# Kernel tuning notes

Measured on AMD Instinct MI355X. Metric: run time of the kernel, lower is better.

## Reference

```python
import jax, jax.numpy as jnp
import numpy as np

# NTU-25 joint groupings (0-indexed)
BODY_GROUP = [np.array([5,6,7,8,22,23])-1, np.array([9,10,11,12,24,25])-1,
              np.array([13,14,15,16])-1, np.array([17,18,19,20])-1,
              np.array([1,2,3,4,21])-1]
PART_GROUP = [np.array([1,2,21])-1, np.array([3,4])-1, np.array([5,6,7])-1,
              np.array([8,22,23])-1, np.array([9,10,11])-1, np.array([12,24,25])-1,
              np.array([13,14])-1, np.array([15,16])-1, np.array([17,18])-1,
              np.array([19,20])-1]

def _corr_joints(parts):
    num_joints = max(max(p) for p in parts) + 1
    res = []
    for i in range(num_joints):
        for j, p in enumerate(parts):
            if i in p:
                res.append(j)
                break
    return np.asarray(res, dtype=np.int32)

JOINTS_PART = _corr_joints(PART_GROUP)  # [25] -> part id in [0,10)
JOINTS_BODY = _corr_joints(BODY_GROUP)  # [25] -> body id in [0,5)

N, C, T, V, S = 64, 96, 128, 25, 3

def setup_inputs() -> dict:
    key = jax.random.key(0)
    ks = jax.random.split(key, 10)
    x = jax.random.normal(ks[0], (N, C, T, V), jnp.float32)
    p_att = jax.random.normal(ks[1], (N, S, 10, 10), jnp.float32)
    b_att = jax.random.normal(ks[2], (N, S, 5, 5), jnp.float32)
    w_in = jax.random.normal(ks[3], (3 * C, C), jnp.float32) * (1.0 / np.sqrt(C))
    b_in = jax.random.normal(ks[4], (3 * C,), jnp.float32) * 0.01
    w_ff = jax.random.normal(ks[5], (C, C), jnp.float32) * (1.0 / np.sqrt(C))
    b_ff = jax.random.normal(ks[6], (C,), jnp.float32) * 0.01
    bn_gamma = jnp.ones((C,), jnp.float32)
    bn_beta = jnp.zeros((C,), jnp.float32)
    bn_mean = jnp.zeros((C,), jnp.float32)
    bn_var = jnp.ones((C,), jnp.float32)
    return {"x": x, "p_att": p_att, "b_att": b_att, "w_in": w_in, "b_in": b_in,
            "w_ff": w_ff, "b_ff": b_ff, "bn_gamma": bn_gamma, "bn_beta": bn_beta,
            "bn_mean": bn_mean, "bn_var": bn_var}

def reference(x, p_att, b_att, w_in, b_in, w_ff, b_ff, bn_gamma, bn_beta, bn_mean, bn_var):
    n, c, t, v = x.shape
    s = S
    mid = c // s
    jp = jnp.asarray(JOINTS_PART)
    jb = jnp.asarray(JOINTS_BODY)
    # 1x1 conv -> QKV: [N, 3C, T, V] viewed as [N, 3, S, mid, T, V]
    qkv = jnp.einsum('nctv,oc->notv', x, w_in) + b_in[None, :, None, None]
    qkv = qkv.reshape(n, 3, s, mid, t, v)
    q, k, val = qkv[:, 0], qkv[:, 1], qkv[:, 2]
    att = jnp.tanh(jnp.einsum('nsctu,nsctv->nsuv', q, k) / (mid * t))
    # structured gather of part/body biases to joint-level [N,S,V,V]
    pp = p_att[:, :, jp[:, None], jp[None, :]]
    bb = b_att[:, :, jb[:, None], jb[None, :]]
    att = att + pp + bb
    y = jnp.einsum('nsuv,nsctv->nsctu', att, val).reshape(n, c, t, v)
    # ff_nets: 1x1 conv + BatchNorm (eval mode, running stats)
    y = jnp.einsum('nctv,oc->notv', y, w_ff) + b_ff[None, :, None, None]
    inv = bn_gamma / jnp.sqrt(bn_var + 1e-5)
    y = (y - bn_mean[None, :, None, None]) * inv[None, :, None, None] + bn_beta[None, :, None, None]
    return jax.nn.leaky_relu(x + y, 0.1)
```

## Files before the change

kernel.cpp:

```cpp
#include <hip/hip_runtime.h>
#include <cmath>

#define NN 64
#define CC 96
#define TT 128
#define VV 25
#define SS 3
#define TB 4
#define NTB (TT/TB)
#define ROWS (TB*VV)
#define XTROWS 112

#define XTP 104
#define XFP 104
#define QKP 200
#define VALP 40
#define YLP 104

typedef __attribute__((ext_vector_type(8))) __bf16 bf16x8;
typedef __attribute__((ext_vector_type(4))) float f32x4;

#define MFMA16(a,b,c) __builtin_amdgcn_mfma_f32_16x16x32_bf16((a),(b),(c),0,0,0)

__constant__ int JP[25] = {0,0,1,1,2,2,2,3,4,4,4,5,6,6,7,7,8,8,9,9,0,3,3,5,5};
__constant__ int JB[25] = {4,4,4,4,0,0,0,0,1,1,1,1,2,2,2,2,3,3,3,3,4,0,0,1,1};

__device__ inline unsigned short f2b(float f) {
  unsigned int u = __float_as_uint(f);
  u += 0x7fffu + ((u >> 16) & 1u);
  return (unsigned short)(u >> 16);
}
__device__ inline float b2f(unsigned short h) {
  return __uint_as_float(((unsigned int)h) << 16);
}
__device__ inline bf16x8 ldbf8(const unsigned short* p) {
  union { uint4 u; bf16x8 b; } z;
  z.u = *(const uint4*)p;
  return z.b;
}
__device__ inline f32x4 fz() {
  f32x4 z; z[0] = 0.f; z[1] = 0.f; z[2] = 0.f; z[3] = 0.f; return z;
}

__global__ __launch_bounds__(256) void k0(
    const float* __restrict__ w_in, const float* __restrict__ w_ff,
    const float* __restrict__ b_ff, const float* __restrict__ gam,
    const float* __restrict__ bet, const float* __restrict__ mea,
    const float* __restrict__ var,
    unsigned short* __restrict__ wbin, unsigned short* __restrict__ wbff,
    float* __restrict__ scsh)
{
  int i = blockIdx.x * 256 + threadIdx.x;
  if (i < 288 * 96) wbin[i] = f2b(w_in[i]);
  if (i < 96 * 96)  wbff[i] = f2b(w_ff[i]);
  if (i < 96) {
    float sc = gam[i] * rsqrtf(var[i] + 1e-5f);
    scsh[i]      = sc;
    scsh[96 + i] = (b_ff[i] - mea[i]) * sc + bet[i];
  }
}

__device__ inline void stageA(const float* __restrict__ xb,
                              unsigned short* __restrict__ xf, int tid)
{
  for (int e = tid; e < CC * (ROWS / 4); e += 256) {
    int i4 = e % (ROWS / 4), c = e / (ROWS / 4);
    float4 v = *(const float4*)&xb[(size_t)c * (TT * VV) + i4 * 4];
    ushort4 h;
    h.x = f2b(v.x); h.y = f2b(v.y); h.z = f2b(v.z); h.w = f2b(v.w);
    *(ushort4*)&xf[c * XFP + i4 * 4] = h;
  }
}
__device__ inline void stageB(const unsigned short* __restrict__ xf,
                              unsigned short* __restrict__ xT, int tid)
{
  for (int e = tid; e < ROWS * (CC / 4); e += 256) {
    int i = e % ROWS, c4 = e / ROWS;
    ushort4 h;
    h.x = xf[(c4 * 4 + 0) * XFP + i];
    h.y = xf[(c4 * 4 + 1) * XFP + i];
    h.z = xf[(c4 * 4 + 2) * XFP + i];
    h.w = xf[(c4 * 4 + 3) * XFP + i];
    *(ushort4*)&xT[i * XTP + c4 * 4] = h;
  }
}

__global__ __launch_bounds__(256, 2) void k1(
    const float* __restrict__ x, const unsigned short* __restrict__ wbin,
    const float* __restrict__ b_in, float* __restrict__ partG)
{
  __shared__ __align__(16) unsigned short xT[XTROWS * XTP];
  __shared__ __align__(16) unsigned short qk[XTROWS * QKP];
  __shared__ float bL[192];
  unsigned short* xf = qk;

  const int tid  = threadIdx.x;
  const int wid  = tid >> 6, lane = tid & 63;
  const int lrow = lane & 15;
  const int lk8  = (lane >> 4) << 3;
  const int ldr4 = (lane >> 4) << 2;
  const int tb = blockIdx.x & (NTB - 1);
  const int n  = blockIdx.x >> 5;
  const int t0 = tb * TB;

  const float* xb = x + (size_t)n * CC * TT * VV + (size_t)t0 * VV;
  stageA(xb, xf, tid);
  if (tid < 192) bL[tid] = b_in[tid];
  __syncthreads();
  stageB(xf, xT, tid);
  __syncthreads();

  f32x4 acc[3][7];
  #pragma unroll
  for (int i = 0; i < 3; ++i)
    #pragma unroll
    for (int nf = 0; nf < 7; ++nf) acc[i][nf] = fz();

  #pragma unroll
  for (int ks = 0; ks < 3; ++ks) {
    bf16x8 a[3];
    #pragma unroll
    for (int i = 0; i < 3; ++i)
      a[i] = ldbf8(&wbin[((wid * 3 + i) * 16 + lrow) * 96 + ks * 32 + lk8]);
    #pragma unroll
    for (int nf = 0; nf < 7; ++nf) {
      bf16x8 b = ldbf8(&xT[(nf * 16 + lrow) * XTP + ks * 32 + lk8]);
      #pragma unroll
      for (int i = 0; i < 3; ++i)
        acc[i][nf] = MFMA16(a[i], b, acc[i][nf]);
    }
  }
  #pragma unroll
  for (int i = 0; i < 3; ++i) {
    int ob = (wid * 3 + i) * 16 + ldr4;
    float4 bb = *(const float4*)&bL[ob];
    #pragma unroll
    for (int nf = 0; nf < 7; ++nf) {
      int col = nf * 16 + lrow;
      ushort4 h;
      h.x = f2b(acc[i][nf][0] + bb.x);
      h.y = f2b(acc[i][nf][1] + bb.y);
      h.z = f2b(acc[i][nf][2] + bb.z);
      h.w = f2b(acc[i][nf][3] + bb.w);
      *(ushort4*)&qk[col * QKP + ob] = h;
    }
  }
  __syncthreads();

  if (wid < 3) {
    const int s = wid;
    f32x4 g[2][2];
    g[0][0] = fz(); g[0][1] = fz(); g[1][0] = fz(); g[1][1] = fz();
    #pragma unroll
    for (int dt = 0; dt < TB; ++dt) {
      int r0 = dt * VV;
      bf16x8 a0 = ldbf8(&qk[(r0 + lrow) * QKP + s * 32 + lk8]);
      bf16x8 a1 = ldbf8(&qk[(r0 + 16 + lrow) * QKP + s * 32 + lk8]);
      bf16x8 b0 = ldbf8(&qk[(r0 + lrow) * QKP + 96 + s * 32 + lk8]);
      bf16x8 b1 = ldbf8(&qk[(r0 + 16 + lrow) * QKP + 96 + s * 32 + lk8]);
      g[0][0] = MFMA16(a0, b0, g[0][0]);
      g[0][1] = MFMA16(a0, b1, g[0][1]);
      g[1][0] = MFMA16(a1, b0, g[1][0]);
      g[1][1] = MFMA16(a1, b1, g[1][1]);
    }
    float* pg = partG + ((size_t)tb * (NN * SS) + (n * SS + s)) * (VV * VV);
    #pragma unroll
    for (int mi = 0; mi < 2; ++mi)
      #pragma unroll
      for (int ni = 0; ni < 2; ++ni)
        #pragma unroll
        for (int r = 0; r < 4; ++r) {
          int u = mi * 16 + ldr4 + r, v = ni * 16 + lrow;
          if (u < VV && v < VV) pg[u * VV + v] = g[mi][ni][r];
        }
  }
}

__global__ __launch_bounds__(256) void k2(
    const float* __restrict__ partG, const float* __restrict__ p_att,
    const float* __restrict__ b_att, unsigned short* __restrict__ att)
{
  const int ns = blockIdx.x;
  for (int e = threadIdx.x; e < 1024; e += 256) {
    int u = e >> 5, v = e & 31;
    float a = 0.f;
    if (u < VV && v < VV) {
      float g = 0.f;
      #pragma unroll 4
      for (int tb = 0; tb < NTB; ++tb)
        g += partG[((size_t)tb * (NN * SS) + ns) * (VV * VV) + u * VV + v];
      a = tanhf(g * (1.0f / 4096.0f))
        + p_att[(size_t)ns * 100 + JP[u] * 10 + JP[v]]
        + b_att[(size_t)ns * 25  + JB[u] * 5  + JB[v]];
    }
    att[(size_t)ns * 1024 + e] = f2b(a);
  }
}

__global__ __launch_bounds__(256, 2) void k3(
    const float* __restrict__ x, const unsigned short* __restrict__ wbin,
    const unsigned short* __restrict__ wbff,
    const float* __restrict__ b_in, const float* __restrict__ scsh,
    const unsigned short* __restrict__ att, float* __restrict__ out)
{
  __shared__ __align__(16) unsigned short xT[XTROWS * XTP];
  __shared__ __align__(16) unsigned short val[384 * VALP];
  unsigned short* xf = val;

  const int tid  = threadIdx.x;
  const int wid  = tid >> 6, lane = tid & 63;
  const int lrow = lane & 15;
  const int lk8  = (lane >> 4) << 3;
  const int ldr4 = (lane >> 4) << 2;
  const int tb = blockIdx.x & (NTB - 1);
  const int n  = blockIdx.x >> 5;
  const int t0 = tb * TB;

  const float* xb = x + (size_t)n * CC * TT * VV + (size_t)t0 * VV;
  stageA(xb, xf, tid);
  __syncthreads();
  stageB(xf, xT, tid);
  __syncthreads();
  {
    uint4 z; z.x = 0u; z.y = 0u; z.z = 0u; z.w = 0u;
    for (int e = tid; e < 384; e += 256)
      *(uint4*)&val[e * VALP + 24] = z;
  }
  __syncthreads();

  for (int nf = wid * 2; nf < 7 && nf < wid * 2 + 2; ++nf) {
    f32x4 acc[6];
    #pragma unroll
    for (int mf = 0; mf < 6; ++mf) acc[mf] = fz();
    #pragma unroll
    for (int ks = 0; ks < 3; ++ks) {
      bf16x8 b = ldbf8(&xT[(nf * 16 + lrow) * XTP + ks * 32 + lk8]);
      #pragma unroll
      for (int mf = 0; mf < 6; ++mf) {
        bf16x8 a = ldbf8(&wbin[(192 + mf * 16 + lrow) * 96 + ks * 32 + lk8]);
        acc[mf] = MFMA16(a, b, acc[mf]);
      }
    }
    int col = nf * 16 + lrow;
    if (col < ROWS) {
      int dt = col / VV, v = col - dt * VV;
      #pragma unroll
      for (int mf = 0; mf < 6; ++mf) {
        float4 bb = *(const float4*)&b_in[192 + mf * 16 + ldr4];
        const float* bp = (const float*)&bb;
        #pragma unroll
        for (int r = 0; r < 4; ++r) {
          int c = mf * 16 + ldr4 + r;
          val[(dt * 96 + c) * VALP + v] = f2b(acc[mf][r] + bp[r]);
        }
      }
    }
  }
  __syncthreads();

  const unsigned short* attn = att + (size_t)(n * SS) * 1024;
  f32x4 y[3][2][2];
  #pragma unroll
  for (int s = 0; s < 3; ++s)
    #pragma unroll
    for (int mi = 0; mi < 2; ++mi)
      #pragma unroll
      for (int ci = 0; ci < 2; ++ci) y[s][mi][ci] = fz();

  #pragma unroll
  for (int s = 0; s < 3; ++s) {
    bf16x8 b[2];
    #pragma unroll
    for (int ci = 0; ci < 2; ++ci) {
      int col = (wid * 2 + ci) * 16 + lrow;
      int dt = col >> 5, cm = col & 31;
      b[ci] = ldbf8(&val[(dt * 96 + s * 32 + cm) * VALP + lk8]);
    }
    #pragma unroll
    for (int mi = 0; mi < 2; ++mi) {
      bf16x8 a = ldbf8(&attn[(size_t)s * 1024 + (mi * 16 + lrow) * 32 + lk8]);
      #pragma unroll
      for (int ci = 0; ci < 2; ++ci)
        y[s][mi][ci] = MFMA16(a, b[ci], y[s][mi][ci]);
    }
  }
  __syncthreads();

  unsigned short* yL = val;
  #pragma unroll
  for (int s = 0; s < 3; ++s)
    #pragma unroll
    for (int mi = 0; mi < 2; ++mi)
      #pragma unroll
      for (int ci = 0; ci < 2; ++ci) {
        int col = (wid * 2 + ci) * 16 + lrow;
        int dt = col >> 5, cm = col & 31;
        int c = s * 32 + cm;
        #pragma unroll
        for (int r = 0; r < 4; ++r) {
          int u = mi * 16 + ldr4 + r;
          if (u < VV) yL[(dt * VV + u) * YLP + c] = f2b(y[s][mi][ci][r]);
        }
      }
  __syncthreads();

  for (int nf = wid * 2; nf < 7 && nf < wid * 2 + 2; ++nf) {
    f32x4 acc[6];
    #pragma unroll
    for (int mf = 0; mf < 6; ++mf) acc[mf] = fz();
    #pragma unroll
    for (int ks = 0; ks < 3; ++ks) {
      bf16x8 b = ldbf8(&yL[(nf * 16 + lrow) * YLP + ks * 32 + lk8]);
      #pragma unroll
      for (int mf = 0; mf < 6; ++mf) {
        bf16x8 a = ldbf8(&wbff[(mf * 16 + lrow) * 96 + ks * 32 + lk8]);
        acc[mf] = MFMA16(a, b, acc[mf]);
      }
    }
    int i = nf * 16 + lrow;
    if (i < ROWS) {
      int dt = i / VV, u = i - dt * VV;
      int t = t0 + dt;
      #pragma unroll
      for (int mf = 0; mf < 6; ++mf) {
        int o0 = mf * 16 + ldr4;
        ushort4 xr = *(const ushort4*)&xT[i * XTP + o0];
        float4 sc = *(const float4*)&scsh[o0];
        float4 sh = *(const float4*)&scsh[96 + o0];
        float zr[4];
        zr[0] = acc[mf][0] * sc.x + sh.x + b2f(xr.x);
        zr[1] = acc[mf][1] * sc.y + sh.y + b2f(xr.y);
        zr[2] = acc[mf][2] * sc.z + sh.z + b2f(xr.z);
        zr[3] = acc[mf][3] * sc.w + sh.w + b2f(xr.w);
        #pragma unroll
        for (int r = 0; r < 4; ++r) {
          float z = zr[r];
          z = (z >= 0.f) ? z : 0.1f * z;
          out[((size_t)(n * CC + o0 + r) * TT + t) * VV + u] = z;
        }
      }
    }
  }
}

extern "C" void kernel_launch(void* const* d_in, const int* in_sizes, int n_in,
                              void* d_out, int out_size, void* d_ws, size_t ws_size,
                              hipStream_t stream)
{
  const float* x     = (const float*)d_in[0];
  const float* p_att = (const float*)d_in[1];
  const float* b_att = (const float*)d_in[2];
  const float* w_in  = (const float*)d_in[3];
  const float* b_in  = (const float*)d_in[4];
  const float* w_ff  = (const float*)d_in[5];
  const float* b_ff  = (const float*)d_in[6];
  const float* gam   = (const float*)d_in[7];
  const float* bet   = (const float*)d_in[8];
  const float* mea   = (const float*)d_in[9];
  const float* var   = (const float*)d_in[10];
  float* out = (float*)d_out;

  char* ws = (char*)d_ws;
  unsigned short* wbin = (unsigned short*)ws;
  unsigned short* wbff = wbin + 288 * 96;
  unsigned short* attw = wbff + 96 * 96;
  float* scsh  = (float*)(ws + 466944);
  float* partG = (float*)(ws + 467712);

  k0<<<108, 256, 0, stream>>>(w_in, w_ff, b_ff, gam, bet, mea, var,
                              wbin, wbff, scsh);
  k1<<<NN * NTB, 256, 0, stream>>>(x, wbin, b_in, partG);
  k2<<<NN * SS, 256, 0, stream>>>(partG, p_att, b_att, attw);
  k3<<<NN * NTB, 256, 0, stream>>>(x, wbin, wbff, b_in, scsh, attw, out);
}
```

Baseline: 127.8 us.

## Stage bf16 transposed x in workspace from k1 and reuse it in k3

k1 now also writes a bf16, time-major padded (32 joints x 96 channels) copy of x to workspace. k3 reads that copy straight into MFMA fragments instead of reloading fp32 x, converting and transposing it through shared memory. The value projection and attention stages are re-laid out so val is stored channel-major in a single smaller LDS buffer. The residual now reads fp32 x directly from global memory. This cuts k3's LDS footprint and staging barriers, at the cost of extra global writes in k1 and an extra global read of x in the epilogue.

Result: slower. 133.0 us (+4.1%).

```diff
diff --git a/kernel.cpp b/kernel.cpp
--- a/kernel.cpp
+++ b/kernel.cpp
@@ -14,8 +14,8 @@
 #define XTP 104
 #define XFP 104
 #define QKP 200
-#define VALP 40
-#define YLP 104
+#define VP  132
+#define YP  104
 
 typedef __attribute__((ext_vector_type(8))) __bf16 bf16x8;
 typedef __attribute__((ext_vector_type(4))) float f32x4;
@@ -29,9 +29,6 @@
   unsigned int u = __float_as_uint(f);
   u += 0x7fffu + ((u >> 16) & 1u);
   return (unsigned short)(u >> 16);
-}
-__device__ inline float b2f(unsigned short h) {
-  return __uint_as_float(((unsigned int)h) << 16);
 }
 __device__ inline bf16x8 ldbf8(const unsigned short* p) {
   union { uint4 u; bf16x8 b; } z;
@@ -72,7 +69,8 @@
   }
 }
 __device__ inline void stageB(const unsigned short* __restrict__ xf,
-                              unsigned short* __restrict__ xT, int tid)
+                              unsigned short* __restrict__ xT,
+                              unsigned short* __restrict__ xwp, int tid)
 {
   for (int e = tid; e < ROWS * (CC / 4); e += 256) {
     int i = e % ROWS, c4 = e / ROWS;
@@ -82,12 +80,15 @@
     h.z = xf[(c4 * 4 + 2) * XFP + i];
     h.w = xf[(c4 * 4 + 3) * XFP + i];
     *(ushort4*)&xT[i * XTP + c4 * 4] = h;
+    int dt = i / VV, v = i - dt * VV;
+    *(ushort4*)&xwp[(size_t)(dt * 32 + v) * 96 + c4 * 4] = h;
   }
 }
 
 __global__ __launch_bounds__(256, 2) void k1(
     const float* __restrict__ x, const unsigned short* __restrict__ wbin,
-    const float* __restrict__ b_in, float* __restrict__ partG)
+    const float* __restrict__ b_in, float* __restrict__ partG,
+    unsigned short* __restrict__ xw)
 {
   __shared__ __align__(16) unsigned short xT[XTROWS * XTP];
   __shared__ __align__(16) unsigned short qk[XTROWS * QKP];
@@ -104,10 +105,12 @@
   const int t0 = tb * TB;
 
   const float* xb = x + (size_t)n * CC * TT * VV + (size_t)t0 * VV;
+  unsigned short* xwp = xw + (size_t)(n * TT + t0) * 32 * 96;
+
   stageA(xb, xf, tid);
   if (tid < 192) bL[tid] = b_in[tid];
   __syncthreads();
-  stageB(xf, xT, tid);
+  stageB(xf, xT, xwp, tid);
   __syncthreads();
 
   f32x4 acc[3][7];
@@ -198,14 +201,14 @@
 }
 
 __global__ __launch_bounds__(256, 2) void k3(
-    const float* __restrict__ x, const unsigned short* __restrict__ wbin,
+    const float* __restrict__ x, const unsigned short* __restrict__ xw,
+    const unsigned short* __restrict__ wbin,
     const unsigned short* __restrict__ wbff,
     const float* __restrict__ b_in, const float* __restrict__ scsh,
     const unsigned short* __restrict__ att, float* __restrict__ out)
 {
-  __shared__ __align__(16) unsigned short xT[XTROWS * XTP];
-  __shared__ __align__(16) unsigned short val[384 * VALP];
-  unsigned short* xf = val;
+  __shared__ __align__(16) unsigned short val[96 * VP];
+  unsigned short* yL = val;
 
   const int tid  = threadIdx.x;
   const int wid  = tid >> 6, lane = tid & 63;
@@ -216,127 +219,126 @@
   const int n  = blockIdx.x >> 5;
   const int t0 = tb * TB;
 
-  const float* xb = x + (size_t)n * CC * TT * VV + (size_t)t0 * VV;
-  stageA(xb, xf, tid);
-  __syncthreads();
-  stageB(xf, xT, tid);
-  __syncthreads();
-  {
-    uint4 z; z.x = 0u; z.y = 0u; z.z = 0u; z.w = 0u;
-    for (int e = tid; e < 384; e += 256)
-      *(uint4*)&val[e * VALP + 24] = z;
-  }
-  __syncthreads();
-
-  for (int nf = wid * 2; nf < 7 && nf < wid * 2 + 2; ++nf) {
-    f32x4 acc[6];
-    #pragma unroll
-    for (int mf = 0; mf < 6; ++mf) acc[mf] = fz();
-    #pragma unroll
-    for (int ks = 0; ks < 3; ++ks) {
-      bf16x8 b = ldbf8(&xT[(nf * 16 + lrow) * XTP + ks * 32 + lk8]);
-      #pragma unroll
-      for (int mf = 0; mf < 6; ++mf) {
-        bf16x8 a = ldbf8(&wbin[(192 + mf * 16 + lrow) * 96 + ks * 32 + lk8]);
-        acc[mf] = MFMA16(a, b, acc[mf]);
-      }
-    }
-    int col = nf * 16 + lrow;
-    if (col < ROWS) {
-      int dt = col / VV, v = col - dt * VV;
-      #pragma unroll
-      for (int mf = 0; mf < 6; ++mf) {
-        float4 bb = *(const float4*)&b_in[192 + mf * 16 + ldr4];
-        const float* bp = (const float*)&bb;
-        #pragma unroll
-        for (int r = 0; r < 4; ++r) {
-          int c = mf * 16 + ldr4 + r;
-          val[(dt * 96 + c) * VALP + v] = f2b(acc[mf][r] + bp[r]);
+  const unsigned short* xwn = xw + (size_t)(n * TT + t0) * 32 * 96;
+
+  f32x4 vacc[2][6];
+  #pragma unroll
+  for (int m = 0; m < 2; ++m)
+    #pragma unroll
+    for (int of = 0; of < 6; ++of) vacc[m][of] = fz();
+
+  #pragma unroll
+  for (int ks = 0; ks < 3; ++ks) {
+    bf16x8 bw[6];
+    #pragma unroll
+    for (int of = 0; of < 6; ++of)
+      bw[of] = ldbf8(&wbin[(192 + of * 16 + lrow) * 96 + ks * 32 + lk8]);
+    #pragma unroll
+    for (int m = 0; m < 2; ++m) {
+      bf16x8 a = ldbf8(&xwn[(size_t)((wid + m * 4) * 16 + lrow) * 96 + ks * 32 + lk8]);
+      #pragma unroll
+      for (int of = 0; of < 6; ++of)
+        vacc[m][of] = MFMA16(a, bw[of], vacc[m][of]);
+    }
+  }
+  float bv[6];
+  #pragma unroll
+  for (int of = 0; of < 6; ++of) bv[of] = b_in[192 + of * 16 + lrow];
+
+  #pragma unroll
+  for (int m = 0; m < 2; ++m) {
+    int i0 = (wid + m * 4) * 16 + ldr4;
+    int v0 = i0 & 31;
+    #pragma unroll
+    for (int of = 0; of < 6; ++of) {
+      int cout = of * 16 + lrow;
+      ushort4 h;
+      h.x = (v0 + 0 < VV) ? f2b(vacc[m][of][0] + bv[of]) : (unsigned short)0;
+      h.y = (v0 + 1 < VV) ? f2b(vacc[m][of][1] + bv[of]) : (unsigned short)0;
+      h.z = (v0 + 2 < VV) ? f2b(vacc[m][of][2] + bv[of]) : (unsigned short)0;
+      h.w = (v0 + 3 < VV) ? f2b(vacc[m][of][3] + bv[of]) : (unsigned short)0;
+      *(ushort4*)&val[cout * VP + i0] = h;
+    }
+  }
+  __syncthreads();
+
+  const unsigned short* attn = att + (size_t)n * SS * 1024;
+  f32x4 pacc[3][2][2];
+  #pragma unroll
+  for (int s = 0; s < 3; ++s)
+    #pragma unroll
+    for (int mi = 0; mi < 2; ++mi)
+      #pragma unroll
+      for (int uf = 0; uf < 2; ++uf) pacc[s][mi][uf] = fz();
+
+  #pragma unroll
+  for (int s = 0; s < 3; ++s) {
+    bf16x8 av[2], bu[2];
+    #pragma unroll
+    for (int mi = 0; mi < 2; ++mi)
+      av[mi] = ldbf8(&val[(s * 32 + mi * 16 + lrow) * VP + wid * 32 + lk8]);
+    #pragma unroll
+    for (int uf = 0; uf < 2; ++uf)
+      bu[uf] = ldbf8(&attn[s * 1024 + (uf * 16 + lrow) * 32 + lk8]);
+    #pragma unroll
+    for (int mi = 0; mi < 2; ++mi)
+      #pragma unroll
+      for (int uf = 0; uf < 2; ++uf)
+        pacc[s][mi][uf] = MFMA16(av[mi], bu[uf], pacc[s][mi][uf]);
+  }
+  __syncthreads();
+
+  #pragma unroll
+  for (int s = 0; s < 3; ++s)
+    #pragma unroll
+    for (int mi = 0; mi < 2; ++mi)
+      #pragma unroll
+      for (int uf = 0; uf < 2; ++uf) {
+        int u = uf * 16 + lrow;
+        if (u < VV) {
+          int c0 = s * 32 + mi * 16 + ldr4;
+          ushort4 h;
+          h.x = f2b(pacc[s][mi][uf][0]);
+          h.y = f2b(pacc[s][mi][uf][1]);
+          h.z = f2b(pacc[s][mi][uf][2]);
+          h.w = f2b(pacc[s][mi][uf][3]);
+          *(ushort4*)&yL[(wid * VV + u) * YP + c0] = h;
         }
       }
-    }
-  }
-  __syncthreads();
-
-  const unsigned short* attn = att + (size_t)(n * SS) * 1024;
-  f32x4 y[3][2][2];
-  #pragma unroll
-  for (int s = 0; s < 3; ++s)
-    #pragma unroll
-    for (int mi = 0; mi < 2; ++mi)
-      #pragma unroll
-      for (int ci = 0; ci < 2; ++ci) y[s][mi][ci] = fz();
-
-  #pragma unroll
-  for (int s = 0; s < 3; ++s) {
-    bf16x8 b[2];
-    #pragma unroll
-    for (int ci = 0; ci < 2; ++ci) {
-      int col = (wid * 2 + ci) * 16 + lrow;
-      int dt = col >> 5, cm = col & 31;
-      b[ci] = ldbf8(&val[(dt * 96 + s * 32 + cm) * VALP + lk8]);
-    }
-    #pragma unroll
-    for (int mi = 0; mi < 2; ++mi) {
-      bf16x8 a = ldbf8(&attn[(size_t)s * 1024 + (mi * 16 + lrow) * 32 + lk8]);
-      #pragma unroll
-      for (int ci = 0; ci < 2; ++ci)
-        y[s][mi][ci] = MFMA16(a, b[ci], y[s][mi][ci]);
-    }
-  }
-  __syncthreads();
-
-  unsigned short* yL = val;
-  #pragma unroll
-  for (int s = 0; s < 3; ++s)
-    #pragma unroll
-    for (int mi = 0; mi < 2; ++mi)
-      #pragma unroll
-      for (int ci = 0; ci < 2; ++ci) {
-        int col = (wid * 2 + ci) * 16 + lrow;
-        int dt = col >> 5, cm = col & 31;
-        int c = s * 32 + cm;
+  __syncthreads();
+
+  #pragma unroll
+  for (int rep = 0; rep < 2; ++rep) {
+    int nf = wid + rep * 4;
+    if (nf < 7) {
+      f32x4 facc[6];
+      #pragma unroll
+      for (int of = 0; of < 6; ++of) facc[of] = fz();
+      #pragma unroll
+      for (int ks = 0; ks < 3; ++ks) {
+        bf16x8 by = ldbf8(&yL[(nf * 16 + lrow) * YP + ks * 32 + lk8]);
         #pragma unroll
-        for (int r = 0; r < 4; ++r) {
-          int u = mi * 16 + ldr4 + r;
-          if (u < VV) yL[(dt * VV + u) * YLP + c] = f2b(y[s][mi][ci][r]);
+        for (int of = 0; of < 6; ++of) {
+          bf16x8 aw = ldbf8(&wbff[(of * 16 + lrow) * 96 + ks * 32 + lk8]);
+          facc[of] = MFMA16(aw, by, facc[of]);
         }
       }
-  __syncthreads();
-
-  for (int nf = wid * 2; nf < 7 && nf < wid * 2 + 2; ++nf) {
-    f32x4 acc[6];
-    #pragma unroll
-    for (int mf = 0; mf < 6; ++mf) acc[mf] = fz();
-    #pragma unroll
-    for (int ks = 0; ks < 3; ++ks) {
-      bf16x8 b = ldbf8(&yL[(nf * 16 + lrow) * YLP + ks * 32 + lk8]);
-      #pragma unroll
-      for (int mf = 0; mf < 6; ++mf) {
-        bf16x8 a = ldbf8(&wbff[(mf * 16 + lrow) * 96 + ks * 32 + lk8]);
-        acc[mf] = MFMA16(a, b, acc[mf]);
-      }
-    }
-    int i = nf * 16 + lrow;
-    if (i < ROWS) {
-      int dt = i / VV, u = i - dt * VV;
-      int t = t0 + dt;
-      #pragma unroll
-      for (int mf = 0; mf < 6; ++mf) {
-        int o0 = mf * 16 + ldr4;
-        ushort4 xr = *(const ushort4*)&xT[i * XTP + o0];
-        float4 sc = *(const float4*)&scsh[o0];
-        float4 sh = *(const float4*)&scsh[96 + o0];
-        float zr[4];
-        zr[0] = acc[mf][0] * sc.x + sh.x + b2f(xr.x);
-        zr[1] = acc[mf][1] * sc.y + sh.y + b2f(xr.y);
-        zr[2] = acc[mf][2] * sc.z + sh.z + b2f(xr.z);
-        zr[3] = acc[mf][3] * sc.w + sh.w + b2f(xr.w);
+      int i = nf * 16 + lrow;
+      if (i < ROWS) {
+        size_t base = (size_t)n * CC * (TT * VV) + (size_t)t0 * VV + i;
         #pragma unroll
-        for (int r = 0; r < 4; ++r) {
-          float z = zr[r];
-          z = (z >= 0.f) ? z : 0.1f * z;
-          out[((size_t)(n * CC + o0 + r) * TT + t) * VV + u] = z;
+        for (int of = 0; of < 6; ++of) {
+          int o0 = of * 16 + ldr4;
+          float4 sc = *(const float4*)&scsh[o0];
+          float4 sh = *(const float4*)&scsh[96 + o0];
+          const float* scp = (const float*)&sc;
+          const float* shp = (const float*)&sh;
+          #pragma unroll
+          for (int r = 0; r < 4; ++r) {
+            size_t idx = base + (size_t)(o0 + r) * (TT * VV);
+            float z = facc[of][r] * scp[r] + shp[r] + x[idx];
+            out[idx] = (z >= 0.f) ? z : 0.1f * z;
+          }
         }
       }
     }
@@ -366,10 +368,11 @@
   unsigned short* attw = wbff + 96 * 96;
   float* scsh  = (float*)(ws + 466944);
   float* partG = (float*)(ws + 467712);
+  unsigned short* xw = (unsigned short*)(ws + 15827712);
 
   k0<<<108, 256, 0, stream>>>(w_in, w_ff, b_ff, gam, bet, mea, var,
                               wbin, wbff, scsh);
-  k1<<<NN * NTB, 256, 0, stream>>>(x, wbin, b_in, partG);
+  k1<<<NN * NTB, 256, 0, stream>>>(x, wbin, b_in, partG, xw);
   k2<<<NN * SS, 256, 0, stream>>>(partG, p_att, b_att, attw);
-  k3<<<NN * NTB, 256, 0, stream>>>(x, wbin, wbff, b_in, scsh, attw, out);
-}
+  k3<<<NN * NTB, 256, 0, stream>>>(x, xw, wbin, wbff, b_in, scsh, attw, out);
+}
```
